# Optimization experiments

Measured on AMD Instinct MI355X. Metric: run time of the kernel, lower is better.

## Reference

```python
import jax, jax.numpy as jnp
import numpy as np

D_HEAD = 64
D_MODEL = 1024
N_HEADS = D_MODEL // D_HEAD
MAX_TOKENS = 2048


def setup_inputs() -> dict:
    key = jax.random.key(0)
    ks = jax.random.split(key, 5)
    batch, pos = 2, 2048
    # kaiming_normal_ on (n_heads, d_model, d_head): fan_in = d_model*d_head -> std = sqrt(2/fan_in)
    std_qkv = np.sqrt(2.0 / (D_MODEL * D_HEAD)).astype(np.float32)
    # xavier_normal_ on (d_model, d_model): std = sqrt(2/(fan_in+fan_out))
    std_out = np.sqrt(2.0 / (D_MODEL + D_MODEL)).astype(np.float32)
    return {
        "residual_stream": jax.random.normal(ks[0], (batch, pos, D_MODEL), dtype=jnp.float32),
        "weight_query": jax.random.normal(ks[1], (N_HEADS, D_MODEL, D_HEAD), dtype=jnp.float32) * std_qkv,
        "weight_key": jax.random.normal(ks[2], (N_HEADS, D_MODEL, D_HEAD), dtype=jnp.float32) * std_qkv,
        "weight_value": jax.random.normal(ks[3], (N_HEADS, D_MODEL, D_HEAD), dtype=jnp.float32) * std_qkv,
        "weight_out": jax.random.normal(ks[4], (D_MODEL, D_MODEL), dtype=jnp.float32) * std_out,
    }


def reference(residual_stream, weight_query, weight_key, weight_value, weight_out):
    # QKV projections: [b, p, m] x [h, m, d] -> [b, h, p, d]
    q = jnp.einsum('bpm,hmd->bhpd', residual_stream, weight_query)
    k = jnp.einsum('bpm,hmd->bhpd', residual_stream, weight_key)
    v = jnp.einsum('bpm,hmd->bhpd', residual_stream, weight_value)

    n_tokens = residual_stream.shape[1]
    # scaled scores [b, h, dest, src]
    scores = jnp.einsum('bhqd,bhkd->bhqk', q, k) / jnp.sqrt(jnp.float32(D_HEAD))
    # causal mask: -inf above the diagonal
    causal = jnp.tril(jnp.ones((n_tokens, n_tokens), dtype=bool))
    scores = jnp.where(causal, scores, jnp.float32(-jnp.inf))
    pattern = jax.nn.softmax(scores, axis=-1)

    attn = jnp.einsum('bhqk,bhkd->bhqd', pattern, v)  # [b, h, dest, d_head]
    # concat heads -> [b, p, h*d_head]
    b, h, p, d = attn.shape
    attn_concat = jnp.transpose(attn, (0, 2, 1, 3)).reshape(b, p, h * d)
    return jnp.einsum('bpm,mn->bpn', attn_concat, weight_out)
```

## Files before the change

kernel.cpp:

```cpp
#include <hip/hip_runtime.h>
#include <hip/hip_bf16.h>
#include <stdint.h>


typedef __bf16 bf16x8 __attribute__((ext_vector_type(8)));
typedef float f32x4 __attribute__((ext_vector_type(4)));
typedef unsigned short u16;

__device__ __forceinline__ u16 f2bf(float f) {
  unsigned u = __float_as_uint(f);
  u += 0x7fffu + ((u >> 16) & 1u);
  return (u16)(u >> 16);
}

__global__ __launch_bounds__(256) void xcvt_k(const float* __restrict__ in,
                                              u16* __restrict__ out) {
  int i = (blockIdx.x * 256 + threadIdx.x) * 8;
  float4 f0 = *reinterpret_cast<const float4*>(in + i);
  float4 f1 = *reinterpret_cast<const float4*>(in + i + 4);
  u16 tmp[8] = {f2bf(f0.x), f2bf(f0.y), f2bf(f0.z), f2bf(f0.w),
                f2bf(f1.x), f2bf(f1.y), f2bf(f1.z), f2bf(f1.w)};
  *reinterpret_cast<uint4*>(out + i) = *reinterpret_cast<uint4*>(tmp);
}

__global__ __launch_bounds__(256) void transpose_cvt_k(const float* __restrict__ in,
                                                       u16* __restrict__ out,
                                                       int R, int C) {
  __shared__ u16 tile[64][80];
  int b = blockIdx.z;
  int r0 = blockIdx.x * 64, c0 = blockIdx.y * 64;
  const float* ip = in + (size_t)b * R * C;
  u16* op = out + (size_t)b * R * C;
  int t = threadIdx.x;
  int r = t >> 2, cb = (t & 3) * 16;
  const float4* src = reinterpret_cast<const float4*>(ip + (size_t)(r0 + r) * C + c0 + cb);
  u16 tmp[16];
#pragma unroll
  for (int v = 0; v < 4; v++) {
    float4 f = src[v];
    tmp[v * 4 + 0] = f2bf(f.x);
    tmp[v * 4 + 1] = f2bf(f.y);
    tmp[v * 4 + 2] = f2bf(f.z);
    tmp[v * 4 + 3] = f2bf(f.w);
  }
  *reinterpret_cast<uint4*>(&tile[r][cb]) = *reinterpret_cast<uint4*>(&tmp[0]);
  *reinterpret_cast<uint4*>(&tile[r][cb + 8]) = *reinterpret_cast<uint4*>(&tmp[8]);
  __syncthreads();
  int c = t >> 2, rb = (t & 3) * 16;
  uint4 outv[2];
  u16* tp = reinterpret_cast<u16*>(outv);
#pragma unroll
  for (int j = 0; j < 16; j++) tp[j] = tile[rb + j][c];
  uint4* dst = reinterpret_cast<uint4*>(op + (size_t)(c0 + c) * R + r0 + rb);
  dst[0] = outv[0];
  dst[1] = outv[1];
}

__global__ __launch_bounds__(256) void transpose_qkv_k(const float* __restrict__ Wq,
                                                       const float* __restrict__ Wk,
                                                       const float* __restrict__ Wv,
                                                       u16* __restrict__ outBase) {
  __shared__ u16 tile[64][80];
  int z = blockIdx.z;
  int sel = z >> 4, head = z & 15;
  const float* W = (sel == 0) ? Wq : (sel == 1 ? Wk : Wv);
  const float* ip = W + (size_t)head * 65536;
  u16* op = outBase + (size_t)sel * 1048576 + (size_t)head * 65536;
  int r0 = blockIdx.x * 64;
  int t = threadIdx.x;
  int r = t >> 2, cb = (t & 3) * 16;
  const float4* src = reinterpret_cast<const float4*>(ip + (size_t)(r0 + r) * 64 + cb);
  u16 tmp[16];
#pragma unroll
  for (int v = 0; v < 4; v++) {
    float4 f = src[v];
    tmp[v * 4 + 0] = f2bf(f.x);
    tmp[v * 4 + 1] = f2bf(f.y);
    tmp[v * 4 + 2] = f2bf(f.z);
    tmp[v * 4 + 3] = f2bf(f.w);
  }
  *reinterpret_cast<uint4*>(&tile[r][cb]) = *reinterpret_cast<uint4*>(&tmp[0]);
  *reinterpret_cast<uint4*>(&tile[r][cb + 8]) = *reinterpret_cast<uint4*>(&tmp[8]);
  __syncthreads();
  int c = t >> 2, rb = (t & 3) * 16;
  uint4 outv[2];
  u16* tp = reinterpret_cast<u16*>(outv);
#pragma unroll
  for (int j = 0; j < 16; j++) tp[j] = tile[rb + j][c];
  uint4* dst = reinterpret_cast<uint4*>(op + (size_t)c * 1024 + r0 + rb);
  dst[0] = outv[0];
  dst[1] = outv[1];
}

__device__ __forceinline__ void gemm128_core(const u16* __restrict__ A,
                                             const u16* __restrict__ BT,
                                             int m0, int n0,
                                             f32x4 (&acc)[4][4]) {
  __shared__ u16 As[128][72];
  __shared__ u16 Bs[128][72];
  int t = threadIdx.x, l = t & 63;
  int w = t >> 6, wm = w & 1, wn = w >> 1;
  int l15 = l & 15, q4 = l >> 4;
  int sr = t >> 1, sch = (t & 1) * 32;
  f32x4 z4 = {0.f, 0.f, 0.f, 0.f};
#pragma unroll
  for (int mi = 0; mi < 4; mi++)
#pragma unroll
    for (int nt = 0; nt < 4; nt++) acc[mi][nt] = z4;

  for (int k0 = 0; k0 < 1024; k0 += 64) {
    __syncthreads();
    {
      const uint4* sa = reinterpret_cast<const uint4*>(A + (size_t)(m0 + sr) * 1024 + k0 + sch);
      const uint4* sb = reinterpret_cast<const uint4*>(BT + (size_t)(n0 + sr) * 1024 + k0 + sch);
      uint4 a0 = sa[0], a1 = sa[1], a2 = sa[2], a3 = sa[3];
      uint4 b0 = sb[0], b1 = sb[1], b2 = sb[2], b3 = sb[3];
      uint4* da = reinterpret_cast<uint4*>(&As[sr][sch]);
      da[0] = a0; da[1] = a1; da[2] = a2; da[3] = a3;
      uint4* db = reinterpret_cast<uint4*>(&Bs[sr][sch]);
      db[0] = b0; db[1] = b1; db[2] = b2; db[3] = b3;
    }
    __syncthreads();
#pragma unroll
    for (int kk = 0; kk < 2; kk++) {
      bf16x8 af[4], bfr[4];
#pragma unroll
      for (int mi = 0; mi < 4; mi++)
        af[mi] = *reinterpret_cast<const bf16x8*>(&As[wm * 64 + mi * 16 + l15][kk * 32 + q4 * 8]);
#pragma unroll
      for (int nt = 0; nt < 4; nt++)
        bfr[nt] = *reinterpret_cast<const bf16x8*>(&Bs[wn * 64 + nt * 16 + l15][kk * 32 + q4 * 8]);
#pragma unroll
      for (int mi = 0; mi < 4; mi++)
#pragma unroll
        for (int nt = 0; nt < 4; nt++)
          acc[mi][nt] = __builtin_amdgcn_mfma_f32_16x16x32_bf16(af[mi], bfr[nt], acc[mi][nt], 0, 0, 0);
    }
  }
}

__global__ __launch_bounds__(256) void qkv_gemm128_k(const u16* __restrict__ A,
                                                     const u16* __restrict__ BT,
                                                     u16* __restrict__ Q,
                                                     u16* __restrict__ K,
                                                     u16* __restrict__ VT2) {
  const float QSCALE = 0.125f * 1.44269504088896340736f;
  int m0 = blockIdx.x * 128, n0 = blockIdx.y * 128;
  f32x4 acc[4][4];
  gemm128_core(A, BT, m0, n0, acc);
  int t = threadIdx.x, l = t & 63;
  int w = t >> 6, wm = w & 1, wn = w >> 1;
  int l15 = l & 15, q4 = l >> 4;
#pragma unroll
  for (int mi = 0; mi < 4; mi++) {
#pragma unroll
    for (int nt = 0; nt < 4; nt++) {
#pragma unroll
      for (int r = 0; r < 4; r++) {
        int m = m0 + wm * 64 + mi * 16 + q4 * 4 + r;
        int n = n0 + wn * 64 + nt * 16 + l15;
        int wsel = n >> 10, h = (n >> 6) & 15, d = n & 63;
        int b = m >> 11, p = m & 2047;
        size_t bh = (size_t)(b * 16 + h);
        float v = acc[mi][nt][r];
        if (wsel == 0)
          Q[(bh * 2048 + p) * 64 + d] = f2bf(v * QSCALE);
        else if (wsel == 1)
          K[(bh * 2048 + p) * 64 + d] = f2bf(v);
        else
          VT2[((bh * 32 + (p >> 6)) * 64 + d) * 64 + (p & 63)] = f2bf(v);
      }
    }
  }
}

__global__ __launch_bounds__(256) void out_gemm128_k(const u16* __restrict__ A,
                                                     const u16* __restrict__ BT,
                                                     float* __restrict__ O) {
  int m0 = blockIdx.x * 128, n0 = blockIdx.y * 128;
  f32x4 acc[4][4];
  gemm128_core(A, BT, m0, n0, acc);
  int t = threadIdx.x, l = t & 63;
  int w = t >> 6, wm = w & 1, wn = w >> 1;
  int l15 = l & 15, q4 = l >> 4;
#pragma unroll
  for (int mi = 0; mi < 4; mi++) {
#pragma unroll
    for (int nt = 0; nt < 4; nt++) {
#pragma unroll
      for (int r = 0; r < 4; r++) {
        int m = m0 + wm * 64 + mi * 16 + q4 * 4 + r;
        int n = n0 + wn * 64 + nt * 16 + l15;
        O[(size_t)m * 1024 + n] = acc[mi][nt][r];
      }
    }
  }
}

__global__ __launch_bounds__(256) void attn_k(const u16* __restrict__ Q,
                                              const u16* __restrict__ K,
                                              const u16* __restrict__ VT2,
                                              u16* __restrict__ A) {
  __shared__ u16 Ks[64][72];
  __shared__ u16 Vs[64][72];
  __shared__ u16 P[4][16][80];
  int pr = blockIdx.x, h = blockIdx.y, b = blockIdx.z;
  size_t bh = (size_t)(b * 16 + h);
  const u16* Qp = Q + bh * 2048 * 64;
  const u16* Kp = K + bh * 2048 * 64;
  const u16* Vt = VT2 + bh * 32 * 64 * 64;
  int t = threadIdx.x, l = t & 63, w = t >> 6;
  int l15 = l & 15, q4 = l >> 4;
  const float NEG = -1e30f;
  f32x4 z4 = {0.f, 0.f, 0.f, 0.f};
  int srow = (t & 127) >> 1, shalf = t & 1;
  bool isV = t >= 128;

#pragma unroll
  for (int which = 0; which < 2; which++) {
    int qt = which ? (31 - pr) : pr;
    int qrow = qt * 64 + w * 16 + l15;
    bf16x8 qf0 = *reinterpret_cast<const bf16x8*>(Qp + (size_t)qrow * 64 + q4 * 8);
    bf16x8 qf1 = *reinterpret_cast<const bf16x8*>(Qp + (size_t)qrow * 64 + 32 + q4 * 8);

    f32x4 accO[4] = {z4, z4, z4, z4};
    float rs[4] = {0.f, 0.f, 0.f, 0.f};

    for (int kt = 0; kt <= qt; kt++) {
      __syncthreads();
      {
        const u16* src = isV ? (Vt + ((size_t)kt * 64 + srow) * 64 + shalf * 32)
                             : (Kp + ((size_t)(kt * 64 + srow)) * 64 + shalf * 32);
        const uint4* s4 = reinterpret_cast<const uint4*>(src);
        uint4 v0 = s4[0], v1 = s4[1], v2 = s4[2], v3 = s4[3];
        uint4* d4 = isV ? reinterpret_cast<uint4*>(&Vs[srow][shalf * 32])
                        : reinterpret_cast<uint4*>(&Ks[srow][shalf * 32]);
        d4[0] = v0; d4[1] = v1; d4[2] = v2; d4[3] = v3;
      }
      __syncthreads();

      f32x4 s[4] = {z4, z4, z4, z4};
#pragma unroll
      for (int kk = 0; kk < 2; kk++) {
        bf16x8 qa = (kk == 0) ? qf0 : qf1;
#pragma unroll
        for (int nt = 0; nt < 4; nt++) {
          bf16x8 kf = *reinterpret_cast<const bf16x8*>(&Ks[nt * 16 + l15][kk * 32 + q4 * 8]);
          s[nt] = __builtin_amdgcn_mfma_f32_16x16x32_bf16(qa, kf, s[nt], 0, 0, 0);
        }
      }
      if (kt == qt) {
        int rowl = w * 16 + q4 * 4;
#pragma unroll
        for (int nt = 0; nt < 4; nt++)
#pragma unroll
          for (int r = 0; r < 4; r++)
            if (nt * 16 + l15 > rowl + r) s[nt][r] = NEG;
      }
#pragma unroll
      for (int nt = 0; nt < 4; nt++)
#pragma unroll
        for (int r = 0; r < 4; r++) {
          float p = exp2f(s[nt][r]);
          rs[r] += p;
          P[w][q4 * 4 + r][nt * 16 + l15] = f2bf(p);
        }
#pragma unroll
      for (int kk = 0; kk < 2; kk++) {
        bf16x8 pa = *reinterpret_cast<const bf16x8*>(&P[w][l15][kk * 32 + q4 * 8]);
#pragma unroll
        for (int nt = 0; nt < 4; nt++) {
          bf16x8 vf = *reinterpret_cast<const bf16x8*>(&Vs[nt * 16 + l15][kk * 32 + q4 * 8]);
          accO[nt] = __builtin_amdgcn_mfma_f32_16x16x32_bf16(pa, vf, accO[nt], 0, 0, 0);
        }
      }
    }
#pragma unroll
    for (int r = 0; r < 4; r++) {
#pragma unroll
      for (int sh = 1; sh < 16; sh <<= 1) rs[r] += __shfl_xor(rs[r], sh, 64);
      float inv = 1.f / rs[r];
      int prow = qt * 64 + w * 16 + q4 * 4 + r;
      size_t base = ((size_t)(b * 2048 + prow)) * 1024 + h * 64;
#pragma unroll
      for (int nt = 0; nt < 4; nt++) A[base + nt * 16 + l15] = f2bf(accO[nt][r] * inv);
    }
  }
}

extern "C" void kernel_launch(void* const* d_in, const int* in_sizes, int n_in,
                              void* d_out, int out_size, void* d_ws, size_t ws_size,
                              hipStream_t stream) {
  const float* X  = (const float*)d_in[0];
  const float* Wq = (const float*)d_in[1];
  const float* Wk = (const float*)d_in[2];
  const float* Wv = (const float*)d_in[3];
  const float* Wo = (const float*)d_in[4];
  float* out = (float*)d_out;

  u16* ws = (u16*)d_ws;
  u16* WqT = ws;
  u16* WoT = WqT + 3145728;
  u16* Xb  = WoT + 1048576;
  u16* Qb  = Xb + 4194304;
  u16* Kb  = Qb + 4194304;
  u16* VT2 = Kb + 4194304;
  u16* Ab  = Xb;

  xcvt_k<<<dim3(2048), 256, 0, stream>>>(X, Xb);
  transpose_qkv_k<<<dim3(16, 1, 48), 256, 0, stream>>>(Wq, Wk, Wv, WqT);
  transpose_cvt_k<<<dim3(16, 16, 1), 256, 0, stream>>>(Wo, WoT, 1024, 1024);

  qkv_gemm128_k<<<dim3(32, 24), 256, 0, stream>>>(Xb, WqT, Qb, Kb, VT2);
  attn_k<<<dim3(16, 16, 2), 256, 0, stream>>>(Qb, Kb, VT2, Ab);
  out_gemm128_k<<<dim3(32, 8), 256, 0, stream>>>(Ab, WoT, out);
}
```

Baseline: 207.6 us.

## Double-buffer K/V tiles in attention with register prefetch and MFMA priority

Adds double-buffered shared-memory K/V tiles so that the next tile's global loads are issued into registers before the current tile's MFMAs and written to the other buffer afterward. This cuts the per-iteration syncs from two to one and lets global memory latency overlap with compute. It also raises wave priority around the MFMA blocks and shrinks the P row padding from 80 to 72. In exchange, LDS use and register pressure go up, and the smaller padding may change bank-conflict behaviour.

```diff
diff --git a/kernel.cpp b/kernel.cpp
--- a/kernel.cpp
+++ b/kernel.cpp
@@ -201,9 +201,9 @@
                                               const u16* __restrict__ K,
                                               const u16* __restrict__ VT2,
                                               u16* __restrict__ A) {
-  __shared__ u16 Ks[64][72];
-  __shared__ u16 Vs[64][72];
-  __shared__ u16 P[4][16][80];
+  __shared__ u16 Ks[2][64][72];
+  __shared__ u16 Vs[2][64][72];
+  __shared__ u16 P[4][16][72];
   int pr = blockIdx.x, h = blockIdx.y, b = blockIdx.z;
   size_t bh = (size_t)(b * 16 + h);
   const u16* Qp = Q + bh * 2048 * 64;
@@ -215,6 +215,7 @@
   f32x4 z4 = {0.f, 0.f, 0.f, 0.f};
   int srow = (t & 127) >> 1, shalf = t & 1;
   bool isV = t >= 128;
+  const u16* sbase = (isV ? Vt : Kp) + (size_t)srow * 64 + shalf * 32;
 
 #pragma unroll
   for (int which = 0; which < 2; which++) {
@@ -226,29 +227,36 @@
     f32x4 accO[4] = {z4, z4, z4, z4};
     float rs[4] = {0.f, 0.f, 0.f, 0.f};
 
+    {
+      const uint4* s4 = reinterpret_cast<const uint4*>(sbase);
+      uint4 v0 = s4[0], v1 = s4[1], v2 = s4[2], v3 = s4[3];
+      uint4* d4 = isV ? reinterpret_cast<uint4*>(&Vs[0][srow][shalf * 32])
+                      : reinterpret_cast<uint4*>(&Ks[0][srow][shalf * 32]);
+      d4[0] = v0; d4[1] = v1; d4[2] = v2; d4[3] = v3;
+    }
+    __syncthreads();
+
     for (int kt = 0; kt <= qt; kt++) {
-      __syncthreads();
-      {
-        const u16* src = isV ? (Vt + ((size_t)kt * 64 + srow) * 64 + shalf * 32)
-                             : (Kp + ((size_t)(kt * 64 + srow)) * 64 + shalf * 32);
-        const uint4* s4 = reinterpret_cast<const uint4*>(src);
-        uint4 v0 = s4[0], v1 = s4[1], v2 = s4[2], v3 = s4[3];
-        uint4* d4 = isV ? reinterpret_cast<uint4*>(&Vs[srow][shalf * 32])
-                        : reinterpret_cast<uint4*>(&Ks[srow][shalf * 32]);
-        d4[0] = v0; d4[1] = v1; d4[2] = v2; d4[3] = v3;
-      }
-      __syncthreads();
+      int cur = kt & 1;
+      bool more = kt < qt;
+      uint4 n0, n1, n2, n3;
+      if (more) {
+        const uint4* s4 = reinterpret_cast<const uint4*>(sbase + (size_t)(kt + 1) * 4096);
+        n0 = s4[0]; n1 = s4[1]; n2 = s4[2]; n3 = s4[3];
+      }
 
       f32x4 s[4] = {z4, z4, z4, z4};
+      __builtin_amdgcn_s_setprio(1);
 #pragma unroll
       for (int kk = 0; kk < 2; kk++) {
         bf16x8 qa = (kk == 0) ? qf0 : qf1;
 #pragma unroll
         for (int nt = 0; nt < 4; nt++) {
-          bf16x8 kf = *reinterpret_cast<const bf16x8*>(&Ks[nt * 16 + l15][kk * 32 + q4 * 8]);
+          bf16x8 kf = *reinterpret_cast<const bf16x8*>(&Ks[cur][nt * 16 + l15][kk * 32 + q4 * 8]);
           s[nt] = __builtin_amdgcn_mfma_f32_16x16x32_bf16(qa, kf, s[nt], 0, 0, 0);
         }
       }
+      __builtin_amdgcn_s_setprio(0);
       if (kt == qt) {
         int rowl = w * 16 + q4 * 4;
 #pragma unroll
@@ -265,15 +273,24 @@
           rs[r] += p;
           P[w][q4 * 4 + r][nt * 16 + l15] = f2bf(p);
         }
+      __builtin_amdgcn_s_setprio(1);
 #pragma unroll
       for (int kk = 0; kk < 2; kk++) {
         bf16x8 pa = *reinterpret_cast<const bf16x8*>(&P[w][l15][kk * 32 + q4 * 8]);
 #pragma unroll
         for (int nt = 0; nt < 4; nt++) {
-          bf16x8 vf = *reinterpret_cast<const bf16x8*>(&Vs[nt * 16 + l15][kk * 32 + q4 * 8]);
+          bf16x8 vf = *reinterpret_cast<const bf16x8*>(&Vs[cur][nt * 16 + l15][kk * 32 + q4 * 8]);
           accO[nt] = __builtin_amdgcn_mfma_f32_16x16x32_bf16(pa, vf, accO[nt], 0, 0, 0);
         }
       }
+      __builtin_amdgcn_s_setprio(0);
+
+      if (more) {
+        uint4* d4 = isV ? reinterpret_cast<uint4*>(&Vs[cur ^ 1][srow][shalf * 32])
+                        : reinterpret_cast<uint4*>(&Ks[cur ^ 1][srow][shalf * 32]);
+        d4[0] = n0; d4[1] = n1; d4[2] = n2; d4[3] = n3;
+      }
+      __syncthreads();
     }
 #pragma unroll
     for (int r = 0; r < 4; r++) {
```

Result: no change. 205.3 us (-1.1%).
